# Optimization experiments

Measured on AMD Instinct MI355X. Metric: run time of the kernel, lower is better.

The kernel has to match this reference:

```python
import jax, jax.numpy as jnp
import numpy as np

B, T, N, M, G = 4, 16, 256, 128, 8
D, H, FFN, FD = 512, 8, 1024, 256
HD = D // H
SCALE = HD ** -0.5
EPS = 1e-5
NL = 6  # num_layers; layer 0 has no self-attn


def _ln(x, g, b):
    mu = x.mean(-1, keepdims=True)
    var = ((x - mu) ** 2).mean(-1, keepdims=True)
    return (x - mu) * jax.lax.rsqrt(var + EPS) * g + b


def setup_inputs() -> dict:
    key = jax.random.key(0)
    ks = jax.random.split(key, 16)
    w = lambda i, shape: jax.random.normal(ks[i], shape, jnp.float32) * 0.02
    return {
        'current_tokens': jax.random.normal(ks[0], (B, T, N, D), jnp.float32),
        'trajectory_tokens': jax.random.normal(ks[1], (G, M, D), jnp.float32),
        'sa_in_w': w(2, (NL - 1, 3 * D, D)), 'sa_in_b': jnp.zeros((NL - 1, 3 * D), jnp.float32),
        'sa_out_w': w(3, (NL - 1, D, D)), 'sa_out_b': jnp.zeros((NL - 1, D), jnp.float32),
        'n1_g': jnp.ones((NL - 1, D), jnp.float32), 'n1_b': jnp.zeros((NL - 1, D), jnp.float32),
        'ca_qw': w(4, (NL, D, D)), 'ca_qb': jnp.zeros((NL, D), jnp.float32),
        'ca_kw': w(5, (NL, D, D)), 'ca_kb': jnp.zeros((NL, D), jnp.float32),
        'ca_vw': w(6, (NL, D, D)), 'ca_vb': jnp.zeros((NL, D), jnp.float32),
        'ca_ow': w(7, (NL, D, D)), 'ca_ob': jnp.zeros((NL, D), jnp.float32),
        'n2_g': jnp.ones((NL, D), jnp.float32), 'n2_b': jnp.zeros((NL, D), jnp.float32),
        'f_w1': w(8, (NL, FFN, D)), 'f_b1': jnp.zeros((NL, FFN), jnp.float32),
        'f_w2': w(9, (NL, D, FFN)), 'f_b2': jnp.zeros((NL, D), jnp.float32),
        'n3_g': jnp.ones((NL, D), jnp.float32), 'n3_b': jnp.zeros((NL, D), jnp.float32),
        'out_w': w(10, (FD, D)), 'out_b': jnp.zeros((FD,), jnp.float32),
        'on_g': jnp.ones((FD,), jnp.float32), 'on_b': jnp.zeros((FD,), jnp.float32),
    }


def reference(current_tokens, trajectory_tokens, sa_in_w, sa_in_b, sa_out_w, sa_out_b,
              n1_g, n1_b, ca_qw, ca_qb, ca_kw, ca_kb, ca_vw, ca_vb, ca_ow, ca_ob,
              n2_g, n2_b, f_w1, f_b1, f_w2, f_b2, n3_g, n3_b, out_w, out_b, on_g, on_b):
    x = current_tokens
    attn_list = []
    for i in range(NL):
        if i >= 1:  # self-attention over detections within each frame
            j = i - 1
            xf = x.reshape(B * T, N, D)
            qkv = xf @ sa_in_w[j].T + sa_in_b[j]
            q, k, v = jnp.split(qkv, 3, axis=-1)
            q = q.reshape(B * T, N, H, HD)
            k = k.reshape(B * T, N, H, HD)
            v = v.reshape(B * T, N, H, HD)
            s = jnp.einsum('bnhd,bmhd->bhnm', q, k) * SCALE
            a = jax.nn.softmax(s, axis=-1)
            o = jnp.einsum('bhnm,bmhd->bnhd', a, v).reshape(B * T, N, D)
            o = o @ sa_out_w[j].T + sa_out_b[j]
            x = _ln(x + o.reshape(B, T, N, D), n1_g[j], n1_b[j])
        # cross-attention against group-averaged trajectory memory
        Q = (x @ ca_qw[i].T + ca_qb[i]).reshape(B, T, N, H, HD)
        K = (trajectory_tokens @ ca_kw[i].T + ca_kb[i]).reshape(G, M, H, HD).mean(0)  # (M,H,HD)
        V = (trajectory_tokens @ ca_vw[i].T + ca_vb[i]).reshape(G, M, H, HD).mean(0)
        s = jnp.einsum('btnhd,mhd->btnhm', Q, K) * SCALE
        # current_times=None => rel_pe_mask is zeros(T,M): no future mask; rel_pe bias is dead code in source
        a = jax.nn.softmax(s, axis=-1)  # (B,T,N,H,M)
        o = jnp.einsum('btnhm,mhd->btnhd', a, V).reshape(B, T, N, D)
        o = o @ ca_ow[i].T + ca_ob[i]
        x = _ln(x + o, n2_g[i], n2_b[i])
        # FFN
        h = jax.nn.relu(x @ f_w1[i].T + f_b1[i]) @ f_w2[i].T + f_b2[i]
        x = _ln(x + h, n3_g[i], n3_b[i])
        attn_list.append(a.mean(axis=2))  # (B,T,H,M) avg over detections
    out = _ln(x @ out_w.T + out_b, on_g, on_b)
    return out, jnp.stack(attn_list)
```

## Files before the change

### kernel.cpp

```cpp
#include <hip/hip_runtime.h>
#include <cstdint>
#include <cstddef>

#define Bb 4
#define Tt 16
#define Nn 256
#define Mm 128
#define Gg 8
#define Dd 512
#define Hh 8
#define FFNf 1024
#define FDf 256
#define HDd 64
#define NLl 6
#define SCALEf 0.125f
#define EPSf 1e-5f

typedef __attribute__((ext_vector_type(8))) short short8;
typedef __attribute__((ext_vector_type(4))) float float4_;
typedef __attribute__((ext_vector_type(16))) float f32x16;
typedef __attribute__((ext_vector_type(4))) int int4_;
typedef __attribute__((ext_vector_type(2))) int int2_;

__device__ inline float b2f(ushort u){ union{uint i; float f;} v; v.i = ((uint)u)<<16; return v.f; }
__device__ inline ushort f2b(float f){ union{float f; uint i;} v; v.f=f; uint r = v.i + 0x7fffu + ((v.i>>16)&1u); return (ushort)(r>>16); }
__device__ inline void unpack2(uint w, float& lo, float& hi){
  union{uint i; float f;} a,b; a.i = w<<16; b.i = w & 0xffff0000u; lo=a.f; hi=b.f;
}
__device__ inline float wred(float v){
  #pragma unroll
  for(int m=32;m>=1;m>>=1) v += __shfl_xor(v, m, 64);
  return v;
}
__device__ inline f32x16 zero16(){
  f32x16 z;
  #pragma unroll
  for(int r=0;r<16;r++) z[r]=0.f;
  return z;
}
__device__ inline int xcd_swz(int orig, int nwg){
  int q = nwg >> 3, r = nwg & 7;
  int x = orig & 7, idx = orig >> 3;
  return (x < r ? x*(q+1) : r*(q+1) + (x-r)*q) + idx;
}

__global__ __launch_bounds__(256) void cvt_f2b(const float* __restrict__ in, ushort* __restrict__ out, int n){
  int i = (blockIdx.x*256 + threadIdx.x)*4;
  if (i+3 < n){
    float4_ v = *(const float4_*)(in+i);
    ushort o[4] = {f2b(v[0]),f2b(v[1]),f2b(v[2]),f2b(v[3])};
    *(int2_*)(out+i) = *(const int2_*)o;
  } else {
    for (; i<n; i++) out[i]=f2b(in[i]);
  }
}

__global__ __launch_bounds__(256) void tmean_k(const float* __restrict__ traj, ushort* __restrict__ tm){
  int idx = blockIdx.x*256 + threadIdx.x;
  float s = 0.f;
  #pragma unroll
  for(int g=0; g<8; g++) s += traj[g*65536 + idx];
  tm[idx] = f2b(s*0.125f);
}

template<int RELU>
__global__ __launch_bounds__(256) void gemm_bias(
    const ushort* __restrict__ A, const ushort* __restrict__ W,
    const float* __restrict__ bias, ushort* __restrict__ C,
    int Ndim, int K, int nbx)
{
  __shared__ ushort As[128*64];
  __shared__ ushort Bs[128*64];
  const int wg = xcd_swz(blockIdx.x, gridDim.x);
  const int bn = wg % nbx, bm = wg / nbx;
  const int tid = threadIdx.x;
  const int wid = tid>>6, lane = tid&63;
  const int wr = wid>>1, wc = wid&1;
  const int l15 = lane & 15, l4 = lane >> 4;
  const int rowA0 = bm*128, colB0 = bn*128;

  const ushort* gA[4]; const ushort* gB[4];
  ushort* lA[4]; ushort* lB[4];
  #pragma unroll
  for (int s=0;s<4;s++){
    int q = wid*256 + s*64 + lane;
    int row = q>>3, sl = (q&7)^(row&7);
    gA[s] = A + (size_t)(rowA0+row)*K + sl*8;
    gB[s] = W + (size_t)(colB0+row)*K + sl*8;
    lA[s] = As + (size_t)(wid*256 + s*64)*8;
    lB[s] = Bs + (size_t)(wid*256 + s*64)*8;
  }

  float4_ acc[4][4];
  #pragma unroll
  for(int i=0;i<4;i++)
    #pragma unroll
    for(int j=0;j<4;j++){ acc[i][j][0]=0.f; acc[i][j][1]=0.f; acc[i][j][2]=0.f; acc[i][j][3]=0.f; }

  for (int k0 = 0; k0 < K; k0 += 64) {
    #pragma unroll
    for (int s=0;s<4;s++){
      __builtin_amdgcn_global_load_lds((const unsigned int*)gA[s], (unsigned int*)lA[s], 16, 0, 0);
      __builtin_amdgcn_global_load_lds((const unsigned int*)gB[s], (unsigned int*)lB[s], 16, 0, 0);
      gA[s] += 64; gB[s] += 64;
    }
    __syncthreads();
    #pragma unroll
    for (int kk=0;kk<2;kk++){
      short8 fa[4], fb[4];
      #pragma unroll
      for(int m=0;m<4;m++){
        int r = wr*64 + m*16 + l15;
        fa[m] = *(const short8*)&As[r*64 + (((kk*4 + l4) ^ (r&7))*8)];
      }
      #pragma unroll
      for(int n=0;n<4;n++){
        int r = wc*64 + n*16 + l15;
        fb[n] = *(const short8*)&Bs[r*64 + (((kk*4 + l4) ^ (r&7))*8)];
      }
      #pragma unroll
      for(int m=0;m<4;m++)
        #pragma unroll
        for(int n=0;n<4;n++)
          acc[m][n] = __builtin_amdgcn_mfma_f32_16x16x32_bf16(fa[m], fb[n], acc[m][n], 0,0,0);
    }
    __syncthreads();
  }
  #pragma unroll
  for(int m=0;m<4;m++){
    int grow = rowA0 + wr*64 + m*16 + l4*4;
    #pragma unroll
    for(int n=0;n<4;n++){
      int gcol = colB0 + wc*64 + n*16 + l15;
      float bv = bias[gcol];
      #pragma unroll
      for(int r=0;r<4;r++){
        float v = acc[m][n][r] + bv;
        if (RELU) v = fmaxf(v, 0.f);
        C[(size_t)(grow + r)*Ndim + gcol] = f2b(v);
      }
    }
  }
}

template<int NKEYS, int WRITE_ATTN, int KPF>
__global__ __launch_bounds__(256) void attn_mfma(
  const ushort* __restrict__ Qb, int qstr,
  const ushort* __restrict__ Kb, int kstr,
  const ushort* __restrict__ Vb, int vstr,
  ushort* __restrict__ Ob,
  float* __restrict__ attn_out)
{
  constexpr int NK2 = NKEYS*2;
  __shared__ __align__(16) ushort KsV[NKEYS*64 + 64*NKEYS];
  __shared__ float psum[4][NKEYS];
  const int f = blockIdx.x, h = blockIdx.y;
  const int tid = threadIdx.x, lane = tid & 63, w = tid >> 6;
  const int l31 = lane & 31, l5 = lane >> 5;
  const int swz = (lane & 7) << 4;

  ushort* Ks = KsV;
  ushort* Vt = KsV + NKEYS*64;
  const ushort* kp0 = Kb + (size_t)(KPF ? f*256 : 0)*kstr + h*64;
  const ushort* vp0 = Vb + (size_t)(KPF ? f*256 : 0)*vstr + h*64;

  for (int c = tid; c < NKEYS*8; c += 256){
    int m = c>>3, dc = c&7;
    short8 k8 = *(const short8*)(kp0 + (size_t)m*kstr + dc*8);
    short8 v8 = *(const short8*)(vp0 + (size_t)m*vstr + dc*8);
    *(short8*)((char*)Ks + m*128 + ((dc*16) ^ ((m&7)<<4))) = k8;
    #pragma unroll
    for (int j=0;j<8;j++){
      int d = dc*8 + j;
      *(ushort*)((char*)Vt + d*NK2 + ((m*2) ^ (j<<4))) = (ushort)v8[j];
    }
  }

  short8 qb[2][4];
  const int q0 = w*64;
  const ushort* qp0 = Qb + (size_t)(f*256)*qstr + h*64;
  #pragma unroll
  for (int qj=0;qj<2;qj++)
    #pragma unroll
    for (int dc=0;dc<4;dc++)
      qb[qj][dc] = *(const short8*)(qp0 + (size_t)(q0 + qj*32 + l31)*qstr + dc*16 + l5*8);
  __syncthreads();

  f32x16 O[2][2];
  O[0][0]=zero16(); O[0][1]=zero16(); O[1][0]=zero16(); O[1][1]=zero16();
  float lpart[2] = {0.f, 0.f};

  for (int t = 0; t < NKEYS/32; t++){
    const int k0 = t*32;
    short8 ka[4];
    #pragma unroll
    for (int dc=0;dc<4;dc++)
      ka[dc] = *(const short8*)((char*)Ks + (k0+l31)*128 + (((dc*32) + (l5*16)) ^ swz));
    f32x16 s0 = zero16(), s1 = zero16();
    #pragma unroll
    for (int dc=0;dc<4;dc++){
      s0 = __builtin_amdgcn_mfma_f32_32x32x16_bf16(ka[dc], qb[0][dc], s0, 0,0,0);
      s1 = __builtin_amdgcn_mfma_f32_32x32x16_bf16(ka[dc], qb[1][dc], s1, 0,0,0);
    }
    uint pw[2][8];
    #pragma unroll
    for (int qj=0;qj<2;qj++){
      const f32x16& sv = qj ? s1 : s0;
      float p[16]; float lp = 0.f;
      #pragma unroll
      for (int r=0;r<16;r++){ p[r] = __expf(sv[r]*SCALEf); lp += p[r]; }
      lpart[qj] += lp;
      #pragma unroll
      for (int k=0;k<8;k++){
        uint w_;
        asm("v_cvt_pk_bf16_f32 %0, %1, %2" : "=v"(w_) : "v"(p[2*k]), "v"(p[2*k+1]));
        pw[qj][k] = w_;
      }
    }
    short8 pa[2][2];
    #pragma unroll
    for (int qj=0;qj<2;qj++){
      #pragma unroll
      for (int mj=0;mj<2;mj++){
        uint a0 = pw[qj][mj*4+2], b0 = pw[qj][mj*4+0];
        uint a1 = pw[qj][mj*4+3], b1 = pw[qj][mj*4+1];
        asm("v_permlane32_swap_b32 %0, %1" : "+v"(a0), "+v"(b0));
        asm("v_permlane32_swap_b32 %0, %1" : "+v"(a1), "+v"(b1));
        union { uint u[4]; short8 s8; } u_;
        u_.u[0]=b0; u_.u[1]=b1; u_.u[2]=a0; u_.u[3]=a1;
        pa[qj][mj] = u_.s8;
      }
    }
    #pragma unroll
    for (int mj=0;mj<2;mj++){
      short8 vbf[2];
      #pragma unroll
      for (int dj=0;dj<2;dj++)
        vbf[dj] = *(const short8*)((char*)Vt + (dj*32+l31)*NK2 + (((k0 + mj*16 + l5*8)*2) ^ swz));
      #pragma unroll
      for (int qj=0;qj<2;qj++)
        #pragma unroll
        for (int dj=0;dj<2;dj++)
          O[qj][dj] = __builtin_amdgcn_mfma_f32_32x32x16_bf16(pa[qj][mj], vbf[dj], O[qj][dj], 0,0,0);
    }
  }

  float invl[2];
  #pragma unroll
  for (int qj=0;qj<2;qj++){
    float lt = lpart[qj] + __shfl_xor(lpart[qj], 32, 64);
    invl[qj] = 1.f / lt;
  }

  ushort* op0 = Ob + (size_t)(f*256)*512 + h*64;
  #pragma unroll
  for (int qj=0;qj<2;qj++){
    #pragma unroll
    for (int r=0;r<16;r++){
      int qr = (r&3) + 8*(r>>2) + 4*l5;
      float il = __shfl(invl[qj], (lane & 32) | qr, 64);
      #pragma unroll
      for (int dj=0;dj<2;dj++){
        float v = O[qj][dj][r] * il;
        op0[(size_t)(q0 + qj*32 + qr)*512 + dj*32 + l31] = f2b(v);
      }
    }
  }

  if (WRITE_ATTN){
    for (int t = 0; t < NKEYS/32; t++){
      const int k0 = t*32;
      short8 ka[4];
      #pragma unroll
      for (int dc=0;dc<4;dc++)
        ka[dc] = *(const short8*)((char*)Ks + (k0+l31)*128 + (((dc*32) + (l5*16)) ^ swz));
      f32x16 s0 = zero16(), s1 = zero16();
      #pragma unroll
      for (int dc=0;dc<4;dc++){
        s0 = __builtin_amdgcn_mfma_f32_32x32x16_bf16(ka[dc], qb[0][dc], s0, 0,0,0);
        s1 = __builtin_amdgcn_mfma_f32_32x32x16_bf16(ka[dc], qb[1][dc], s1, 0,0,0);
      }
      float tsum[16];
      #pragma unroll
      for (int r=0;r<16;r++){
        float v = __expf(s0[r]*SCALEf)*invl[0] + __expf(s1[r]*SCALEf)*invl[1];
        #pragma unroll
        for (int mk=1; mk<=16; mk<<=1) v += __shfl_xor(v, mk, 64);
        tsum[r] = v;
      }
      if (l31 == 0){
        #pragma unroll
        for (int r=0;r<16;r++)
          psum[w][k0 + (r&3) + 8*(r>>2) + 4*l5] = tsum[r];
      }
    }
    __syncthreads();
    for (int m = tid; m < NKEYS; m += 256){
      attn_out[f*(Hh*NKEYS) + h*NKEYS + m] =
        (psum[0][m]+psum[1][m]+psum[2][m]+psum[3][m]) * (1.0f/256.0f);
    }
  }
}

__global__ __launch_bounds__(256) void ln_res(
  const ushort* __restrict__ X, const ushort* __restrict__ Oin,
  const float* __restrict__ g, const float* __restrict__ b,
  ushort* __restrict__ Y)
{
  const int row = blockIdx.x*4 + (threadIdx.x>>6);
  const int lane = threadIdx.x & 63;
  const ushort* xp = X + (size_t)row*512 + lane*8;
  const ushort* op = Oin + (size_t)row*512 + lane*8;
  uint xw[4], ow[4];
  *(int4_*)xw = *(const int4_*)xp;
  *(int4_*)ow = *(const int4_*)op;
  float v[8];
  #pragma unroll
  for(int j=0;j<4;j++){
    float xl,xh,ol,oh; unpack2(xw[j],xl,xh); unpack2(ow[j],ol,oh);
    v[2*j] = xl+ol; v[2*j+1] = xh+oh;
  }
  float s=0.f, sq=0.f;
  #pragma unroll
  for(int j=0;j<8;j++){ s += v[j]; sq += v[j]*v[j]; }
  s = wred(s); sq = wred(sq);
  float mu = s * (1.0f/512.0f);
  float var = sq * (1.0f/512.0f) - mu*mu;
  float rs = rsqrtf(var + EPSf);
  ushort ob[8];
  #pragma unroll
  for(int j=0;j<8;j++){
    float gg = g[lane*8+j], bb = b[lane*8+j];
    ob[j] = f2b((v[j]-mu)*rs*gg + bb);
  }
  *(int4_*)(Y + (size_t)row*512 + lane*8) = *(const int4_*)ob;
}

__global__ __launch_bounds__(256) void ln_out(
  const ushort* __restrict__ A, const float* __restrict__ g,
  const float* __restrict__ b, float* __restrict__ out)
{
  const int row = blockIdx.x*4 + (threadIdx.x>>6);
  const int lane = threadIdx.x & 63;
  uint aw[2];
  *(int2_*)aw = *(const int2_*)(A + (size_t)row*256 + lane*4);
  float v[4];
  unpack2(aw[0], v[0], v[1]); unpack2(aw[1], v[2], v[3]);
  float s=0.f, sq=0.f;
  #pragma unroll
  for(int j=0;j<4;j++){ s += v[j]; sq += v[j]*v[j]; }
  s = wred(s); sq = wred(sq);
  float mu = s * (1.0f/256.0f);
  float var = sq * (1.0f/256.0f) - mu*mu;
  float rs = rsqrtf(var + EPSf);
  float4_ o;
  #pragma unroll
  for(int j=0;j<4;j++){
    o[j] = (v[j]-mu)*rs*g[lane*4+j] + b[lane*4+j];
  }
  *(float4_*)(out + (size_t)row*256 + lane*4) = o;
}

static inline void cvt(const float* src, ushort* dst, int n, hipStream_t stream){
  cvt_f2b<<<(n/4 + 255)/256, 256, 0, stream>>>(src, dst, n);
}

extern "C" void kernel_launch(void* const* d_in, const int* in_sizes, int n_in,
                              void* d_out, int out_size, void* d_ws, size_t ws_size,
                              hipStream_t stream) {
  const float* cur      = (const float*)d_in[0];
  const float* traj     = (const float*)d_in[1];
  const float* sa_in_w  = (const float*)d_in[2];
  const float* sa_in_b  = (const float*)d_in[3];
  const float* sa_out_w = (const float*)d_in[4];
  const float* sa_out_b = (const float*)d_in[5];
  const float* n1_g     = (const float*)d_in[6];
  const float* n1_b     = (const float*)d_in[7];
  const float* ca_qw    = (const float*)d_in[8];
  const float* ca_qb    = (const float*)d_in[9];
  const float* ca_kw    = (const float*)d_in[10];
  const float* ca_kb    = (const float*)d_in[11];
  const float* ca_vw    = (const float*)d_in[12];
  const float* ca_vb    = (const float*)d_in[13];
  const float* ca_ow    = (const float*)d_in[14];
  const float* ca_ob    = (const float*)d_in[15];
  const float* n2_g     = (const float*)d_in[16];
  const float* n2_b     = (const float*)d_in[17];
  const float* f_w1     = (const float*)d_in[18];
  const float* f_b1     = (const float*)d_in[19];
  const float* f_w2     = (const float*)d_in[20];
  const float* f_b2     = (const float*)d_in[21];
  const float* n3_g     = (const float*)d_in[22];
  const float* n3_b     = (const float*)d_in[23];
  const float* out_w    = (const float*)d_in[24];
  const float* out_b    = (const float*)d_in[25];
  const float* on_g     = (const float*)d_in[26];
  const float* on_b     = (const float*)d_in[27];

  float* out      = (float*)d_out;
  float* attn_out = out + (size_t)Bb*Tt*Nn*FDf;

  uint8_t* ws = (uint8_t*)d_ws;
  size_t off = 0;
  auto alloc = [&](size_t bytes)->uint8_t*{ uint8_t* p = ws + off; off += (bytes + 255) & ~(size_t)255; return p; };
  ushort* X   = (ushort*)alloc(16777216);
  ushort* B1  = (ushort*)alloc(50331648);
  ushort* B2  = (ushort*)alloc(16777216);
  ushort* Km  = (ushort*)alloc(131072);
  ushort* Vm  = (ushort*)alloc(131072);
  ushort* tm  = (ushort*)alloc(131072);
  ushort* w_sa_in  = (ushort*)alloc((size_t)5*1536*512*2);
  ushort* w_sa_out = (ushort*)alloc((size_t)5*512*512*2);
  ushort* w_ca_q   = (ushort*)alloc((size_t)6*512*512*2);
  ushort* w_ca_k   = (ushort*)alloc((size_t)6*512*512*2);
  ushort* w_ca_v   = (ushort*)alloc((size_t)6*512*512*2);
  ushort* w_ca_o   = (ushort*)alloc((size_t)6*512*512*2);
  ushort* w_f1     = (ushort*)alloc((size_t)6*1024*512*2);
  ushort* w_f2     = (ushort*)alloc((size_t)6*512*1024*2);
  ushort* w_out    = (ushort*)alloc((size_t)256*512*2);

  cvt(cur,      X,        16384*512, stream);
  cvt(sa_in_w,  w_sa_in,  5*1536*512, stream);
  cvt(sa_out_w, w_sa_out, 5*512*512, stream);
  cvt(ca_qw,    w_ca_q,   6*512*512, stream);
  cvt(ca_kw,    w_ca_k,   6*512*512, stream);
  cvt(ca_vw,    w_ca_v,   6*512*512, stream);
  cvt(ca_ow,    w_ca_o,   6*512*512, stream);
  cvt(f_w1,     w_f1,     6*1024*512, stream);
  cvt(f_w2,     w_f2,     6*512*1024, stream);
  cvt(out_w,    w_out,    256*512, stream);
  tmean_k<<<256,256,0,stream>>>(traj, tm);

  for (int i=0;i<NLl;i++){
    if (i>=1){
      int j = i-1;
      gemm_bias<0><<<12*128,256,0,stream>>>(X, w_sa_in + (size_t)j*1536*512, sa_in_b + j*1536, B1, 1536, 512, 12);
      attn_mfma<256,0,1><<<dim3(64,8),256,0,stream>>>(B1, 1536, B1+512, 1536, B1+1024, 1536, B2, nullptr);
      gemm_bias<0><<<4*128,256,0,stream>>>(B2, w_sa_out + (size_t)j*262144, sa_out_b + j*512, B1, 512, 512, 4);
      ln_res<<<4096,256,0,stream>>>(X, B1, n1_g + j*512, n1_b + j*512, X);
    }
    gemm_bias<0><<<4*128,256,0,stream>>>(X, w_ca_q + (size_t)i*262144, ca_qb + i*512, B2, 512, 512, 4);
    gemm_bias<0><<<4,256,0,stream>>>(tm, w_ca_k + (size_t)i*262144, ca_kb + i*512, Km, 512, 512, 4);
    gemm_bias<0><<<4,256,0,stream>>>(tm, w_ca_v + (size_t)i*262144, ca_vb + i*512, Vm, 512, 512, 4);
    attn_mfma<128,1,0><<<dim3(64,8),256,0,stream>>>(B2, 512, Km, 512, Vm, 512, B1, attn_out + (size_t)i*65536);
    gemm_bias<0><<<4*128,256,0,stream>>>(B1, w_ca_o + (size_t)i*262144, ca_ob + i*512, B2, 512, 512, 4);
    ln_res<<<4096,256,0,stream>>>(X, B2, n2_g + i*512, n2_b + i*512, X);
    gemm_bias<1><<<8*128,256,0,stream>>>(X, w_f1 + (size_t)i*524288, f_b1 + i*1024, B1, 1024, 512, 8);
    gemm_bias<0><<<4*128,256,0,stream>>>(B1, w_f2 + (size_t)i*524288, f_b2 + i*512, B2, 512, 1024, 4);
    ln_res<<<4096,256,0,stream>>>(X, B2, n3_g + i*512, n3_b + i*512, X);
  }
  gemm_bias<0><<<2*128,256,0,stream>>>(X, w_out, out_b, B2, 256, 512, 2);
  ln_out<<<4096,256,0,stream>>>(B2, on_g, on_b, out);
}
```

Before: 1.366 ms.

## Double-buffer GEMM LDS tiles with K=32 steps and batch all cross-attn K/V projections

The GEMM core now stages K in 32-wide slices into two LDS buffers, prefetching the next slice while MFMAs consume the current one, and keeps one barrier per iteration instead of two. The LDS layout is reorganised so each warp reads a contiguous half-row region, and launch bounds request 4 blocks per CU for higher occupancy. The per-layer tiny K and V projection GEMMs (4 blocks each) are replaced by a single 48-block kernel computing all layers' K/V up front, cutting 12 poorly parallel launches. The shorter K step halves MFMAs per barrier, which may lower per-iteration efficiency.

```diff
diff --git a/kernel.cpp b/kernel.cpp
--- a/kernel.cpp
+++ b/kernel.cpp
@@ -64,31 +64,29 @@
 }
 
 template<int RELU>
-__global__ __launch_bounds__(256) void gemm_bias(
+__device__ __forceinline__ void gemm_core(
     const ushort* __restrict__ A, const ushort* __restrict__ W,
     const float* __restrict__ bias, ushort* __restrict__ C,
-    int Ndim, int K, int nbx)
-{
-  __shared__ ushort As[128*64];
-  __shared__ ushort Bs[128*64];
-  const int wg = xcd_swz(blockIdx.x, gridDim.x);
-  const int bn = wg % nbx, bm = wg / nbx;
+    int Ndim, int K, int rowA0, int colB0,
+    ushort* As, ushort* Bs)
+{
   const int tid = threadIdx.x;
   const int wid = tid>>6, lane = tid&63;
   const int wr = wid>>1, wc = wid&1;
   const int l15 = lane & 15, l4 = lane >> 4;
-  const int rowA0 = bm*128, colB0 = bn*128;
-
-  const ushort* gA[4]; const ushort* gB[4];
-  ushort* lA[4]; ushort* lB[4];
-  #pragma unroll
-  for (int s=0;s<4;s++){
-    int q = wid*256 + s*64 + lane;
-    int row = q>>3, sl = (q&7)^(row&7);
-    gA[s] = A + (size_t)(rowA0+row)*K + sl*8;
-    gB[s] = W + (size_t)(colB0+row)*K + sl*8;
-    lA[s] = As + (size_t)(wid*256 + s*64)*8;
-    lB[s] = Bs + (size_t)(wid*256 + s*64)*8;
+
+  const ushort* gA[2]; const ushort* gB[2];
+  int ldsOff[2];
+  #pragma unroll
+  for (int s=0;s<2;s++){
+    int p = wid*128 + s*64 + lane;
+    int lrow = p>>3, x = p&7;
+    int logical = x ^ (lrow&7);
+    int row = (logical>>2)*64 + lrow;
+    int ls = logical&3;
+    gA[s] = A + (size_t)(rowA0+row)*K + ls*8;
+    gB[s] = W + (size_t)(colB0+row)*K + ls*8;
+    ldsOff[s] = wid*1024 + s*512;
   }
 
   float4_ acc[4][4];
@@ -97,35 +95,47 @@
     #pragma unroll
     for(int j=0;j<4;j++){ acc[i][j][0]=0.f; acc[i][j][1]=0.f; acc[i][j][2]=0.f; acc[i][j][3]=0.f; }
 
-  for (int k0 = 0; k0 < K; k0 += 64) {
-    #pragma unroll
-    for (int s=0;s<4;s++){
-      __builtin_amdgcn_global_load_lds((const unsigned int*)gA[s], (unsigned int*)lA[s], 16, 0, 0);
-      __builtin_amdgcn_global_load_lds((const unsigned int*)gB[s], (unsigned int*)lB[s], 16, 0, 0);
-      gA[s] += 64; gB[s] += 64;
-    }
-    __syncthreads();
-    #pragma unroll
-    for (int kk=0;kk<2;kk++){
-      short8 fa[4], fb[4];
-      #pragma unroll
-      for(int m=0;m<4;m++){
-        int r = wr*64 + m*16 + l15;
-        fa[m] = *(const short8*)&As[r*64 + (((kk*4 + l4) ^ (r&7))*8)];
-      }
-      #pragma unroll
-      for(int n=0;n<4;n++){
-        int r = wc*64 + n*16 + l15;
-        fb[n] = *(const short8*)&Bs[r*64 + (((kk*4 + l4) ^ (r&7))*8)];
-      }
-      #pragma unroll
-      for(int m=0;m<4;m++)
-        #pragma unroll
-        for(int n=0;n<4;n++)
-          acc[m][n] = __builtin_amdgcn_mfma_f32_16x16x32_bf16(fa[m], fb[n], acc[m][n], 0,0,0);
-    }
-    __syncthreads();
-  }
+  const int NT = K >> 5;
+  #pragma unroll
+  for (int s=0;s<2;s++){
+    __builtin_amdgcn_global_load_lds((const unsigned int*)gA[s], (unsigned int*)(As + ldsOff[s]), 16, 0, 0);
+    __builtin_amdgcn_global_load_lds((const unsigned int*)gB[s], (unsigned int*)(Bs + ldsOff[s]), 16, 0, 0);
+    gA[s] += 32; gB[s] += 32;
+  }
+  __syncthreads();
+
+  int cur = 0;
+  for (int t=0; t<NT; ++t){
+    if (t+1 < NT){
+      #pragma unroll
+      for (int s=0;s<2;s++){
+        __builtin_amdgcn_global_load_lds((const unsigned int*)gA[s], (unsigned int*)(As + (cur^1)*4096 + ldsOff[s]), 16, 0, 0);
+        __builtin_amdgcn_global_load_lds((const unsigned int*)gB[s], (unsigned int*)(Bs + (cur^1)*4096 + ldsOff[s]), 16, 0, 0);
+        gA[s] += 32; gB[s] += 32;
+      }
+    }
+    const ushort* Apt = As + cur*4096;
+    const ushort* Bpt = Bs + cur*4096;
+    short8 fa[4], fb[4];
+    #pragma unroll
+    for(int m=0;m<4;m++){
+      int lrow = m*16 + l15;
+      fa[m] = *(const short8*)&Apt[lrow*64 + (((wr*4 + l4) ^ (l15&7))*8)];
+    }
+    #pragma unroll
+    for(int n=0;n<4;n++){
+      int lrow = n*16 + l15;
+      fb[n] = *(const short8*)&Bpt[lrow*64 + (((wc*4 + l4) ^ (l15&7))*8)];
+    }
+    #pragma unroll
+    for(int m=0;m<4;m++)
+      #pragma unroll
+      for(int n=0;n<4;n++)
+        acc[m][n] = __builtin_amdgcn_mfma_f32_16x16x32_bf16(fa[m], fb[n], acc[m][n], 0,0,0);
+    if (t+1 < NT) __syncthreads();
+    cur ^= 1;
+  }
+
   #pragma unroll
   for(int m=0;m<4;m++){
     int grow = rowA0 + wr*64 + m*16 + l4*4;
@@ -141,6 +151,36 @@
       }
     }
   }
+}
+
+template<int RELU>
+__global__ __launch_bounds__(256, 4) void gemm_bias(
+    const ushort* __restrict__ A, const ushort* __restrict__ W,
+    const float* __restrict__ bias, ushort* __restrict__ C,
+    int Ndim, int K, int nbx)
+{
+  __shared__ ushort As[8192];
+  __shared__ ushort Bs[8192];
+  const int wg = xcd_swz(blockIdx.x, gridDim.x);
+  const int bn = wg % nbx, bm = wg / nbx;
+  gemm_core<RELU>(A, W, bias, C, Ndim, K, bm*128, bn*128, As, Bs);
+}
+
+__global__ __launch_bounds__(256, 4) void kv_all(
+    const ushort* __restrict__ tm,
+    const ushort* __restrict__ wk, const ushort* __restrict__ wv,
+    const float* __restrict__ bk, const float* __restrict__ bv,
+    ushort* __restrict__ KVm)
+{
+  __shared__ ushort As[8192];
+  __shared__ ushort Bs[8192];
+  const int i = blockIdx.x >> 3;
+  const int r8 = blockIdx.x & 7;
+  const int which = r8 >> 2, bn = r8 & 3;
+  const ushort* W  = (which ? wv : wk) + (size_t)i*262144;
+  const float* bias = (which ? bv : bk) + i*512;
+  ushort* C = KVm + (size_t)(i*2 + which)*65536;
+  gemm_core<0>(tm, W, bias, C, 512, 512, 0, bn*128, As, Bs);
 }
 
 template<int NKEYS, int WRITE_ATTN, int KPF>
@@ -406,8 +446,7 @@
   ushort* X   = (ushort*)alloc(16777216);
   ushort* B1  = (ushort*)alloc(50331648);
   ushort* B2  = (ushort*)alloc(16777216);
-  ushort* Km  = (ushort*)alloc(131072);
-  ushort* Vm  = (ushort*)alloc(131072);
+  ushort* KVm = (ushort*)alloc((size_t)6*2*65536*2);
   ushort* tm  = (ushort*)alloc(131072);
   ushort* w_sa_in  = (ushort*)alloc((size_t)5*1536*512*2);
   ushort* w_sa_out = (ushort*)alloc((size_t)5*512*512*2);
@@ -430,6 +469,7 @@
   cvt(f_w2,     w_f2,     6*512*1024, stream);
   cvt(out_w,    w_out,    256*512, stream);
   tmean_k<<<256,256,0,stream>>>(traj, tm);
+  kv_all<<<48,256,0,stream>>>(tm, w_ca_k, w_ca_v, ca_kb, ca_vb, KVm);
 
   for (int i=0;i<NLl;i++){
     if (i>=1){
@@ -440,9 +480,7 @@
       ln_res<<<4096,256,0,stream>>>(X, B1, n1_g + j*512, n1_b + j*512, X);
     }
     gemm_bias<0><<<4*128,256,0,stream>>>(X, w_ca_q + (size_t)i*262144, ca_qb + i*512, B2, 512, 512, 4);
-    gemm_bias<0><<<4,256,0,stream>>>(tm, w_ca_k + (size_t)i*262144, ca_kb + i*512, Km, 512, 512, 4);
-    gemm_bias<0><<<4,256,0,stream>>>(tm, w_ca_v + (size_t)i*262144, ca_vb + i*512, Vm, 512, 512, 4);
-    attn_mfma<128,1,0><<<dim3(64,8),256,0,stream>>>(B2, 512, Km, 512, Vm, 512, B1, attn_out + (size_t)i*65536);
+    attn_mfma<128,1,0><<<dim3(64,8),256,0,stream>>>(B2, 512, KVm + (size_t)i*131072, 512, KVm + (size_t)i*131072 + 65536, 512, B1, attn_out + (size_t)i*65536);
     gemm_bias<0><<<4*128,256,0,stream>>>(B1, w_ca_o + (size_t)i*262144, ca_ob + i*512, B2, 512, 512, 4);
     ln_res<<<4096,256,0,stream>>>(X, B2, n2_g + i*512, n2_b + i*512, X);
     gemm_bias<1><<<8*128,256,0,stream>>>(X, w_f1 + (size_t)i*524288, f_b1 + i*1024, B1, 1024, 512, 8);
```

Result: faster. 1.260 ms (-7.7%).
